# Kernel tuning notes

Hardware: AMD Instinct MI355X
Metric: run time of the kernel (lower is better)

The kernel has to match this reference:

```python
import jax, jax.numpy as jnp
import numpy as np

B, T, C, H = 4, 2048, 1024, 16


def setup_inputs() -> dict:
    key = jax.random.key(0)
    k0, k1, k2 = jax.random.split(key, 3)
    s = C ** -0.5
    return {
        "x": jax.random.normal(k0, (B, T, C), jnp.float32),
        "Wqkv": jax.random.normal(k1, (C, 3 * C), jnp.float32) * s,
        "bqkv": jnp.zeros((3 * C,), jnp.float32),
        "Wo": jax.random.normal(k2, (C, C), jnp.float32) * s,
        "bo": jnp.zeros((C,), jnp.float32),
        "decoder": 1,
    }


def reference(x, Wqkv, bqkv, Wo, bo, decoder):
    Bx, Tx, Cx = x.shape
    d = Cx // H  # head dim
    qkv = x @ Wqkv + bqkv  # [B,T,3C]
    q, k, v = jnp.split(qkv, 3, axis=-1)
    q = q.reshape(Bx, Tx, H, d).transpose(0, 2, 1, 3)  # [B,H,T,d]
    k = k.reshape(Bx, Tx, H, d).transpose(0, 2, 1, 3)
    v = v.reshape(Bx, Tx, H, d).transpose(0, 2, 1, 3)
    # Source: qk / embd_dim**(-0.5)  ==  qk * sqrt(embd_dim)  (faithful quirk)
    scale = jnp.asarray(Cx ** 0.5, x.dtype)
    qk = jnp.einsum("bhqd,bhkd->bhqk", q, k) * scale  # [B,H,T,T]
    if decoder:  # decoder is a Python int constant
        tril = jnp.tril(jnp.ones((Tx, Tx), bool))
        qk = jnp.where(tril, qk, -jnp.inf)
    attn = jax.nn.softmax(qk, axis=-1)
    out = jnp.einsum("bhqk,bhkd->bhqd", attn, v)  # [B,H,T,d]
    out = out.transpose(0, 2, 1, 3).reshape(Bx, Tx, Cx)
    return out @ Wo + bo
```

## Files before the change

kernel.cpp:

```cpp
#include <hip/hip_runtime.h>
#include <cstdint>
#include <cstddef>

#define T_SEQ 2048
#define CEMB  1024
#define NHEAD 16
#define DHEAD 64

#define QSCALE 46.1662413084468f

typedef __attribute__((ext_vector_type(8))) short bf16x8;
typedef __attribute__((ext_vector_type(4))) float f32x4;

static __device__ __forceinline__ unsigned short f2bf(float x) {
    unsigned u = __builtin_bit_cast(unsigned, x);
    unsigned r = (u + 0x7FFFu + ((u >> 16) & 1u)) >> 16;
    return (unsigned short)r;
}
static __device__ __forceinline__ float bf2f(unsigned short b) {
    unsigned u = ((unsigned)b) << 16;
    return __builtin_bit_cast(float, u);
}

static __device__ __forceinline__ void gload16(const short* gsrc, short* ldsbase) {
    __builtin_amdgcn_global_load_lds(
        (const __attribute__((address_space(1))) void*)gsrc,
        (__attribute__((address_space(3))) void*)ldsbase, 16, 0, 0);
}

__global__ __launch_bounds__(256) void gemm_qk_kernel(
    const float* __restrict__ Af,
    const short* __restrict__ Bh, const short* __restrict__ Bl,
    const float* __restrict__ bias,
    short* __restrict__ Chi, short* __restrict__ Clo, int K)
{
    __shared__ __align__(16) short smem[16384];

    const int tid = threadIdx.x;
    const int w = tid >> 6, l = tid & 63;
    const int lr = l & 15, lg = l >> 4;
    const int wr = w >> 1, wc = w & 1;
    const int row0 = blockIdx.y * 128;
    const int col0 = blockIdx.x * 128;

    f32x4 acc[4][4];
    #pragma unroll
    for (int mt = 0; mt < 4; ++mt)
        #pragma unroll
        for (int nt = 0; nt < 4; ++nt)
            acc[mt][nt] = (f32x4){0.f, 0.f, 0.f, 0.f};

    const int sB0 = w * 128 + l, sB1 = sB0 + 64;
    const size_t bO0 = (size_t)(col0 + (sB0 & 127)) * K + (sB0 >> 7) * 8;
    const size_t bO1 = (size_t)(col0 + (sB1 & 127)) * K + (sB1 >> 7) * 8;
    const short* gB0  = Bh + bO0;  const short* gB1  = Bh + bO1;
    const short* gBl0 = Bl + bO0;  const short* gBl1 = Bl + bO1;
    short* const dB0 = &smem[4096 + (w * 128) * 8];
    short* const dB1 = &smem[4096 + (w * 128 + 64) * 8];

    const int arow = tid >> 1, ahalf = tid & 1;
    const float* gAf = Af + (size_t)(row0 + arow) * K + ahalf * 16;

    for (int kt = 0; kt < K; kt += 32) {
        __syncthreads();
        gload16(gB0 + kt, dB0);
        gload16(gB1 + kt, dB1);
        gload16(gBl0 + kt, dB0 + 8192);
        gload16(gBl1 + kt, dB1 + 8192);
        {
            const float* src = gAf + kt;
            float4 f0 = *(const float4*)(src);
            float4 f1 = *(const float4*)(src + 4);
            float4 f2 = *(const float4*)(src + 8);
            float4 f3 = *(const float4*)(src + 12);
            float xs[16] = {f0.x, f0.y, f0.z, f0.w, f1.x, f1.y, f1.z, f1.w,
                            f2.x, f2.y, f2.z, f2.w, f3.x, f3.y, f3.z, f3.w};
            #pragma unroll
            for (int q = 0; q < 2; ++q) {
                bf16x8 h8, l8;
                #pragma unroll
                for (int e = 0; e < 8; ++e) {
                    float x = xs[q * 8 + e];
                    unsigned u = __builtin_bit_cast(unsigned, x);
                    h8[e] = (short)(unsigned short)(u >> 16);
                    float hf = __builtin_bit_cast(float, u & 0xFFFF0000u);
                    l8[e] = (short)f2bf(x - hf);
                }
                int slot = (ahalf * 2 + q) * 128 + arow;
                *(bf16x8*)&smem[slot * 8] = h8;
                *(bf16x8*)&smem[8192 + slot * 8] = l8;
            }
        }
        __syncthreads();

        const int ao = (lg * 128 + wr * 64 + lr) * 8;
        const int bo = 4096 + (lg * 128 + wc * 64 + lr) * 8;
        bf16x8 ahf[4], alf[4];
        #pragma unroll
        for (int mt = 0; mt < 4; ++mt) {
            ahf[mt] = *(const bf16x8*)&smem[ao + mt * 128];
            alf[mt] = *(const bf16x8*)&smem[8192 + ao + mt * 128];
        }
        #pragma unroll
        for (int nt = 0; nt < 4; ++nt) {
            bf16x8 bhf = *(const bf16x8*)&smem[bo + nt * 128];
            bf16x8 blf = *(const bf16x8*)&smem[8192 + bo + nt * 128];
            #pragma unroll
            for (int mt = 0; mt < 4; ++mt) {
                acc[mt][nt] = __builtin_amdgcn_mfma_f32_16x16x32_bf16(ahf[mt], bhf, acc[mt][nt], 0, 0, 0);
                acc[mt][nt] = __builtin_amdgcn_mfma_f32_16x16x32_bf16(alf[mt], bhf, acc[mt][nt], 0, 0, 0);
                acc[mt][nt] = __builtin_amdgcn_mfma_f32_16x16x32_bf16(ahf[mt], blf, acc[mt][nt], 0, 0, 0);
            }
        }
    }

    #pragma unroll
    for (int mt = 0; mt < 4; ++mt) {
        #pragma unroll
        for (int r = 0; r < 4; ++r) {
            int m = row0 + wr * 64 + mt * 16 + lg * 4 + r;
            #pragma unroll
            for (int nt = 0; nt < 4; ++nt) {
                int n = col0 + wc * 64 + nt * 16 + lr;
                float v = acc[mt][nt][r] + bias[n];
                if (n < 1024) v *= QSCALE;
                unsigned u = __builtin_bit_cast(unsigned, v);
                Chi[(size_t)m * 2048 + n] = (short)(unsigned short)(u >> 16);
                float hf = __builtin_bit_cast(float, u & 0xFFFF0000u);
                Clo[(size_t)m * 2048 + n] = (short)f2bf(v - hf);
            }
        }
    }
}

__global__ __launch_bounds__(256) void gemm_v_kernel(
    const float* __restrict__ Af, const short* __restrict__ Bh,
    const float* __restrict__ bias, short* __restrict__ vt, int K)
{
    __shared__ __align__(16) short smem[17408];

    const int tid = threadIdx.x;
    const int w = tid >> 6, l = tid & 63;
    const int lr = l & 15, lg = l >> 4;
    const int wr = w >> 1, wc = w & 1;
    const int row0 = blockIdx.y * 128;
    const int col0 = blockIdx.x * 128;

    f32x4 acc[4][4];
    #pragma unroll
    for (int mt = 0; mt < 4; ++mt)
        #pragma unroll
        for (int nt = 0; nt < 4; ++nt)
            acc[mt][nt] = (f32x4){0.f, 0.f, 0.f, 0.f};

    const int sB0 = w * 128 + l, sB1 = sB0 + 64;
    const size_t bO0 = (size_t)(col0 + (sB0 & 127)) * K + (sB0 >> 7) * 8;
    const size_t bO1 = (size_t)(col0 + (sB1 & 127)) * K + (sB1 >> 7) * 8;
    const short* gB0 = Bh + bO0;  const short* gB1 = Bh + bO1;
    short* const dB0 = &smem[4096 + (w * 128) * 8];
    short* const dB1 = &smem[4096 + (w * 128 + 64) * 8];

    const int arow = tid >> 1, ahalf = tid & 1;
    const float* gAf = Af + (size_t)(row0 + arow) * K + ahalf * 16;

    for (int kt = 0; kt < K; kt += 32) {
        __syncthreads();
        gload16(gB0 + kt, dB0);
        gload16(gB1 + kt, dB1);
        {
            const float* src = gAf + kt;
            float4 f0 = *(const float4*)(src);
            float4 f1 = *(const float4*)(src + 4);
            float4 f2 = *(const float4*)(src + 8);
            float4 f3 = *(const float4*)(src + 12);
            float xs[16] = {f0.x, f0.y, f0.z, f0.w, f1.x, f1.y, f1.z, f1.w,
                            f2.x, f2.y, f2.z, f2.w, f3.x, f3.y, f3.z, f3.w};
            #pragma unroll
            for (int q = 0; q < 2; ++q) {
                bf16x8 h8;
                #pragma unroll
                for (int e = 0; e < 8; ++e) h8[e] = (short)f2bf(xs[q * 8 + e]);
                int slot = (ahalf * 2 + q) * 128 + arow;
                *(bf16x8*)&smem[slot * 8] = h8;
            }
        }
        __syncthreads();

        const int ao = (lg * 128 + wr * 64 + lr) * 8;
        const int bo = 4096 + (lg * 128 + wc * 64 + lr) * 8;
        bf16x8 ahf[4];
        #pragma unroll
        for (int mt = 0; mt < 4; ++mt)
            ahf[mt] = *(const bf16x8*)&smem[ao + mt * 128];
        #pragma unroll
        for (int nt = 0; nt < 4; ++nt) {
            bf16x8 bhf = *(const bf16x8*)&smem[bo + nt * 128];
            #pragma unroll
            for (int mt = 0; mt < 4; ++mt)
                acc[mt][nt] = __builtin_amdgcn_mfma_f32_16x16x32_bf16(ahf[mt], bhf, acc[mt][nt], 0, 0, 0);
        }
    }

    __syncthreads();
    #pragma unroll
    for (int mt = 0; mt < 4; ++mt) {
        const int tb = wr * 64 + mt * 16 + lg * 4;
        #pragma unroll
        for (int nt = 0; nt < 4; ++nt) {
            const int nl = wc * 64 + nt * 16 + lr;
            float bv = bias[col0 + nl];
            unsigned u0 = (unsigned)f2bf(acc[mt][nt][0] + bv) |
                          ((unsigned)f2bf(acc[mt][nt][1] + bv) << 16);
            unsigned u1 = (unsigned)f2bf(acc[mt][nt][2] + bv) |
                          ((unsigned)f2bf(acc[mt][nt][3] + bv) << 16);
            uint2 uu; uu.x = u0; uu.y = u1;
            *(uint2*)&smem[nl * 136 + tb] = uu;
        }
    }
    __syncthreads();

    const int b  = row0 >> 11;
    const int t0 = row0 & 2047;
    #pragma unroll
    for (int i = 0; i < 8; ++i) {
        int nl = (tid >> 4) + i * 16;
        int t8 = (tid & 15) * 8;
        bf16x8 vv = *(const bf16x8*)&smem[nl * 136 + t8];
        int n = col0 + nl;
        int hh = n >> 6, d = n & 63;
        short* dst = vt + ((size_t)((b * NHEAD + hh) * DHEAD + d)) * T_SEQ + t0 + t8;
        *(bf16x8*)dst = vv;
    }
}

__global__ __launch_bounds__(256) void gemm_proj_kernel(
    const short* __restrict__ Ah, const short* __restrict__ Bh,
    const float* __restrict__ bias, float* __restrict__ Cout, int K, int ldc)
{
    __shared__ __align__(16) short smem[16384];

    const int tid = threadIdx.x;
    const int w = tid >> 6, l = tid & 63;
    const int lr = l & 15, lg = l >> 4;
    const int wr = w >> 1, wc = w & 1;
    const int row0 = blockIdx.y * 128;
    const int col0 = blockIdx.x * 128;

    f32x4 acc[4][4];
    #pragma unroll
    for (int mt = 0; mt < 4; ++mt)
        #pragma unroll
        for (int nt = 0; nt < 4; ++nt)
            acc[mt][nt] = (f32x4){0.f, 0.f, 0.f, 0.f};

    const int s0 = w * 128 + l, s1 = s0 + 64;
    const size_t aoff0 = (size_t)(row0 + (s0 & 127)) * K + (s0 >> 7) * 8;
    const size_t aoff1 = (size_t)(row0 + (s1 & 127)) * K + (s1 >> 7) * 8;
    const size_t boff0 = (size_t)(col0 + (s0 & 127)) * K + (s0 >> 7) * 8;
    const size_t boff1 = (size_t)(col0 + (s1 & 127)) * K + (s1 >> 7) * 8;
    const short* gA0 = Ah + aoff0;  const short* gA1 = Ah + aoff1;
    const short* gB0 = Bh + boff0;  const short* gB1 = Bh + boff1;
    short* const dA0 = &smem[(w * 128) * 8];
    short* const dA1 = &smem[(w * 128 + 64) * 8];
    short* const dB0 = &smem[4096 + (w * 128) * 8];
    short* const dB1 = &smem[4096 + (w * 128 + 64) * 8];

    #define PSTAGE(buf, kt) do {                      \
        gload16(gA0 + (kt), dA0 + (buf) * 8192);      \
        gload16(gA1 + (kt), dA1 + (buf) * 8192);      \
        gload16(gB0 + (kt), dB0 + (buf) * 8192);      \
        gload16(gB1 + (kt), dB1 + (buf) * 8192);      \
    } while (0)

    const int nkt = K / 32;
    PSTAGE(0, 0);
    for (int ti = 0; ti < nkt; ++ti) {
        if (ti + 1 < nkt) {
            PSTAGE((ti + 1) & 1, (ti + 1) * 32);
            asm volatile("s_waitcnt vmcnt(4)" ::: "memory");
        } else {
            asm volatile("s_waitcnt vmcnt(0)" ::: "memory");
        }
        __builtin_amdgcn_s_barrier();
        __builtin_amdgcn_sched_barrier(0);

        const int sb = (ti & 1) * 8192;
        const int ao = sb + (lg * 128 + wr * 64 + lr) * 8;
        const int bo = sb + 4096 + (lg * 128 + wc * 64 + lr) * 8;
        bf16x8 ahf[4];
        #pragma unroll
        for (int mt = 0; mt < 4; ++mt)
            ahf[mt] = *(const bf16x8*)&smem[ao + mt * 128];
        #pragma unroll
        for (int nt = 0; nt < 4; ++nt) {
            bf16x8 bhf = *(const bf16x8*)&smem[bo + nt * 128];
            #pragma unroll
            for (int mt = 0; mt < 4; ++mt)
                acc[mt][nt] = __builtin_amdgcn_mfma_f32_16x16x32_bf16(ahf[mt], bhf, acc[mt][nt], 0, 0, 0);
        }
        __builtin_amdgcn_sched_barrier(0);
        __builtin_amdgcn_s_barrier();
        __builtin_amdgcn_sched_barrier(0);
    }
    #undef PSTAGE

    #pragma unroll
    for (int mt = 0; mt < 4; ++mt) {
        #pragma unroll
        for (int r = 0; r < 4; ++r) {
            int m = row0 + wr * 64 + mt * 16 + lg * 4 + r;
            #pragma unroll
            for (int nt = 0; nt < 4; ++nt) {
                int n = col0 + wc * 64 + nt * 16 + lr;
                Cout[(size_t)m * ldc + n] = acc[mt][nt][r] + bias[n];
            }
        }
    }
}

__global__ __launch_bounds__(256) void transpose_split_kernel(
    const float* __restrict__ src, int nsrc,
    short* __restrict__ hi, short* __restrict__ lo)
{
    __shared__ float tile[64][68];
    const int tid = threadIdx.x;
    const int n0 = blockIdx.x * 64, k0 = blockIdx.y * 64;
    {
        int kr = tid >> 2, cg = tid & 3;
        const float* s = src + (size_t)(k0 + kr) * nsrc + n0 + cg * 16;
        #pragma unroll
        for (int q = 0; q < 4; ++q) {
            float4 f = *(const float4*)(s + q * 4);
            tile[kr][cg * 16 + q * 4 + 0] = f.x;
            tile[kr][cg * 16 + q * 4 + 1] = f.y;
            tile[kr][cg * 16 + q * 4 + 2] = f.z;
            tile[kr][cg * 16 + q * 4 + 3] = f.w;
        }
    }
    __syncthreads();
    {
        int nr = tid >> 2, kg = tid & 3;
        int n = n0 + nr;
        bf16x8 h0, h1, lo0, lo1;
        #pragma unroll
        for (int e = 0; e < 8; ++e) {
            float a = tile[kg * 16 + e][nr];
            float b = tile[kg * 16 + 8 + e][nr];
            unsigned short ha = f2bf(a), hb = f2bf(b);
            h0[e] = (short)ha; h1[e] = (short)hb;
            lo0[e] = (short)f2bf(a - bf2f(ha));
            lo1[e] = (short)f2bf(b - bf2f(hb));
        }
        short* dh = hi + (size_t)n * 1024 + k0 + kg * 16;
        *(bf16x8*)dh = h0;
        *(bf16x8*)(dh + 8) = h1;
        if (lo) {
            short* dl = lo + (size_t)n * 1024 + k0 + kg * 16;
            *(bf16x8*)dl = lo0;
            *(bf16x8*)(dl + 8) = lo1;
        }
    }
}

__global__ __launch_bounds__(256) void attn_mfma_kernel(
    const short* __restrict__ qkhi, const short* __restrict__ qklo,
    const short* __restrict__ vt, short* __restrict__ ctxb)
{
    __shared__ __align__(16) short smem[20480];

    const int tid = threadIdx.x;
    const int w = tid >> 6, l = tid & 63;
    const int lr = l & 15, lg = l >> 4;

    const int bid = blockIdx.x;
    const int p  = bid >> 6;
    const int bh = bid & 63;
    const int h = bh & 15, b = bh >> 4;
    const size_t bT = (size_t)b * T_SEQ;

    const int g0 = w * 128 + l, g1 = g0 + 64;
    const int rg0 = g0 >> 3, rg1 = g1 >> 3;
    const int sc0 = (g0 & 7) ^ (rg0 & 7), sc1 = (g1 & 7) ^ (rg1 & 7);
    short* const dK0 = &smem[(w * 128) * 8];
    short* const dK1 = &smem[(w * 128 + 64) * 8];

    const size_t koff0 = (bT + rg0) * 2048 + 1024 + h * DHEAD + sc0 * 8;
    const size_t koff1 = (bT + rg1) * 2048 + 1024 + h * DHEAD + sc1 * 8;
    const short* const pKh0 = qkhi + koff0;
    const short* const pKh1 = qkhi + koff1;
    const short* const pKl0 = qklo + koff0;
    const short* const pKl1 = qklo + koff1;
    const short* const pV0 = vt + ((size_t)((b * NHEAD + h) * DHEAD) + rg0) * T_SEQ + sc0 * 8;
    const short* const pV1 = vt + ((size_t)((b * NHEAD + h) * DHEAD) + rg1) * T_SEQ + sc1 * 8;

    const int psBase = 16384 + w * 1024;
    const int pwChunk = (lg >> 1);
    const int pwIntra = (lg & 1) * 4;

    for (int half = 0; half < 2; ++half) {
        const int xi = half ? (31 - p) : p;
        const int qw = xi * 64 + w * 16;
        const int nsteps = xi + 1;

        __syncthreads();

        bf16x8 qhi[2], qlo[2];
        #pragma unroll
        for (int kk = 0; kk < 2; ++kk) {
            size_t off = (bT + qw + lr) * 2048 + h * DHEAD + kk * 32 + lg * 8;
            qhi[kk] = *(const bf16x8*)(qkhi + off);
            qlo[kk] = *(const bf16x8*)(qklo + off);
        }
        __builtin_amdgcn_sched_barrier(0);

        gload16(pKh0, dK0);
        gload16(pKh1, dK1);
        gload16(pKl0, dK0 + 4096);
        gload16(pKl1, dK1 + 4096);
        gload16(pV0, dK0 + 8192);
        gload16(pV1, dK1 + 8192);
        {
            int j1 = (nsteps > 1) ? 64 : 0;
            gload16(pV0 + j1, dK0 + 12288);
            gload16(pV1 + j1, dK1 + 12288);
        }

        f32x4 O[4];
        #pragma unroll
        for (int dt = 0; dt < 4; ++dt)
            O[dt] = (f32x4){0.f, 0.f, 0.f, 0.f};
        float mrow = -3.0e38f;
        float lrow = 0.f;

        for (int t = 0; t < nsteps; ++t) {
            const int j0 = t * 64;
            asm volatile("s_waitcnt vmcnt(2)" ::: "memory");
            __builtin_amdgcn_s_barrier();
            __builtin_amdgcn_sched_barrier(0);
            const int vbase = 8192 + (t & 1) * 4096;

            f32x4 St[4];
            __builtin_amdgcn_s_setprio(1);
            #pragma unroll
            for (int ct = 0; ct < 4; ++ct) {
                f32x4 s = (f32x4){0.f, 0.f, 0.f, 0.f};
                #pragma unroll
                for (int kk = 0; kk < 2; ++kk) {
                    int j  = ct * 16 + lr;
                    int ck = kk * 4 + lg;
                    int idx = j * 64 + ((ck ^ (j & 7)) << 3);
                    bf16x8 kh8 = *(bf16x8*)&smem[idx];
                    bf16x8 kl8 = *(bf16x8*)&smem[4096 + idx];
                    s = __builtin_amdgcn_mfma_f32_16x16x32_bf16(kh8, qhi[kk], s, 0, 0, 0);
                    s = __builtin_amdgcn_mfma_f32_16x16x32_bf16(kh8, qlo[kk], s, 0, 0, 0);
                    s = __builtin_amdgcn_mfma_f32_16x16x32_bf16(kl8, qhi[kk], s, 0, 0, 0);
                }
                St[ct] = s;
            }
            __builtin_amdgcn_s_setprio(0);
            #pragma unroll
            for (int ct = 0; ct < 4; ++ct) {
                if (j0 + ct * 16 + 15 > qw) {
                    #pragma unroll
                    for (int r = 0; r < 4; ++r) {
                        int jabs = j0 + ct * 16 + lg * 4 + r;
                        St[ct][r] = (jabs <= qw + lr) ? St[ct][r] : -3.0e38f;
                    }
                }
            }

            float tm = fmaxf(fmaxf(fmaxf(St[0][0], St[0][1]), fmaxf(St[0][2], St[0][3])),
                             fmaxf(fmaxf(St[1][0], St[1][1]), fmaxf(St[1][2], St[1][3])));
            tm = fmaxf(tm, fmaxf(fmaxf(fmaxf(St[2][0], St[2][1]), fmaxf(St[2][2], St[2][3])),
                                 fmaxf(fmaxf(St[3][0], St[3][1]), fmaxf(St[3][2], St[3][3]))));
            tm = fmaxf(tm, __shfl_xor(tm, 16));
            tm = fmaxf(tm, __shfl_xor(tm, 32));

            if (__any(tm > mrow)) {
                float mnew  = fmaxf(mrow, tm);
                float alpha = __builtin_amdgcn_exp2f(mrow - mnew);
                mrow = mnew;
                lrow *= alpha;
                #pragma unroll
                for (int r = 0; r < 4; ++r) {
                    float aO = __shfl(alpha, lg * 4 + r);
                    #pragma unroll
                    for (int dt = 0; dt < 4; ++dt)
                        O[dt][r] *= aO;
                }
            }

            #pragma unroll
            for (int ct = 0; ct < 4; ++ct) {
                float p0 = __builtin_amdgcn_exp2f(St[ct][0] - mrow);
                float p1 = __builtin_amdgcn_exp2f(St[ct][1] - mrow);
                float p2 = __builtin_amdgcn_exp2f(St[ct][2] - mrow);
                float p3 = __builtin_amdgcn_exp2f(St[ct][3] - mrow);
                lrow += (p0 + p1) + (p2 + p3);
                unsigned u0 = (__builtin_bit_cast(unsigned, p0) >> 16) |
                              (__builtin_bit_cast(unsigned, p1) & 0xFFFF0000u);
                unsigned u1 = (__builtin_bit_cast(unsigned, p2) >> 16) |
                              (__builtin_bit_cast(unsigned, p3) & 0xFFFF0000u);
                int chunk = ct * 2 + pwChunk;
                int sidx = psBase + lr * 64 + ((chunk ^ (lr & 7)) << 3) + pwIntra;
                uint2 uu; uu.x = u0; uu.y = u1;
                *(uint2*)&smem[sidx] = uu;
            }

            __builtin_amdgcn_wave_barrier();

            bf16x8 pa[2];
            #pragma unroll
            for (int jk = 0; jk < 2; ++jk) {
                int ck = jk * 4 + lg;
                pa[jk] = *(bf16x8*)&smem[psBase + lr * 64 + ((ck ^ (lr & 7)) << 3)];
            }
            __builtin_amdgcn_s_setprio(1);
            #pragma unroll
            for (int dt = 0; dt < 4; ++dt) {
                #pragma unroll
                for (int jk = 0; jk < 2; ++jk) {
                    int d  = dt * 16 + lr;
                    int ck = jk * 4 + lg;
                    bf16x8 vb = *(bf16x8*)&smem[vbase + d * 64 + ((ck ^ (d & 7)) << 3)];
                    O[dt] = __builtin_amdgcn_mfma_f32_16x16x32_bf16(pa[jk], vb, O[dt], 0, 0, 0);
                }
            }
            __builtin_amdgcn_s_setprio(0);

            __builtin_amdgcn_sched_barrier(0);
            __builtin_amdgcn_s_barrier();
            __builtin_amdgcn_sched_barrier(0);

            if (t + 1 < nsteps) {
                size_t ko = (size_t)(t + 1) * 131072;
                gload16(pKh0 + ko, dK0);
                gload16(pKh1 + ko, dK1);
                gload16(pKl0 + ko, dK0 + 4096);
                gload16(pKl1 + ko, dK1 + 4096);
                int jv = (t + 2 < nsteps) ? (t + 2) : (nsteps - 1);
                short* const dV = &smem[8192 + (t & 1) * 4096];
                gload16(pV0 + jv * 64, dV + (w * 128) * 8);
                gload16(pV1 + jv * 64, dV + (w * 128 + 64) * 8);
            }
        }

        float lsum = lrow + __shfl_xor(lrow, 16);
        lsum += __shfl_xor(lsum, 32);
        #pragma unroll
        for (int r = 0; r < 4; ++r) {
            float lO = __shfl(lsum, lg * 4 + r);
            float inv = 1.0f / lO;
            int row = qw + lg * 4 + r;
            #pragma unroll
            for (int dt = 0; dt < 4; ++dt) {
                int col = h * DHEAD + dt * 16 + lr;
                ctxb[(size_t)(b * T_SEQ + row) * CEMB + col] = (short)f2bf(O[dt][r] * inv);
            }
        }
    }
}

extern "C" void kernel_launch(void* const* d_in, const int* in_sizes, int n_in,
                              void* d_out, int out_size, void* d_ws, size_t ws_size,
                              hipStream_t stream)
{
    const float* x    = (const float*)d_in[0];
    const float* Wqkv = (const float*)d_in[1];
    const float* bqkv = (const float*)d_in[2];
    const float* Wo   = (const float*)d_in[3];
    const float* bo   = (const float*)d_in[4];
    float* out = (float*)d_out;

    char* ws = (char*)d_ws;
    short* qkhi = (short*)ws;
    short* qklo = (short*)(ws + (size_t)(32u << 20));
    short* Vt   = (short*)(ws + (size_t)(64u << 20));
    short* ctxb = (short*)(ws + (size_t)(80u << 20));
    short* WhiT = (short*)(ws + (size_t)(96u << 20));
    short* WloT = (short*)(ws + (size_t)(102u << 20));
    short* WoT  = (short*)(ws + (size_t)(108u << 20));

    transpose_split_kernel<<<dim3(48, 16), 256, 0, stream>>>(Wqkv, 3 * CEMB, WhiT, WloT);
    transpose_split_kernel<<<dim3(16, 16), 256, 0, stream>>>(Wo, CEMB, WoT, nullptr);

    gemm_qk_kernel<<<dim3(16, 64), 256, 0, stream>>>(
        x, WhiT, WloT, bqkv, qkhi, qklo, CEMB);

    gemm_v_kernel<<<dim3(8, 64), 256, 0, stream>>>(
        x, WhiT + (size_t)2048 * 1024, bqkv + 2048, Vt, CEMB);

    attn_mfma_kernel<<<dim3(1024), 256, 0, stream>>>(qkhi, qklo, Vt, ctxb);

    gemm_proj_kernel<<<dim3(8, 64), 256, 0, stream>>>(
        ctxb, WoT, bo, out, CEMB, CEMB);
}
```

Before: 329.6 us.

## Double-buffer B tiles and prefetch A registers in QKV projection GEMM

Restructures the QKV GEMM main loop so the next K-slice of the B operand (hi/lo bf16) is loaded into a second LDS buffer, and the next A floats into registers, while the current slice is being multiplied. Explicit vmcnt/lgkmcnt waits and raw s_barrier calls replace the __syncthreads pair, and s_setprio raises wave priority around the MFMA block. This is meant to hide global-load latency behind MFMA work. In exchange it uses more LDS (48KB instead of 32KB), which may cut occupancy, and it relies on hand-counted waitcnt values being correct.

```diff
diff --git a/kernel.cpp b/kernel.cpp
--- a/kernel.cpp
+++ b/kernel.cpp
@@ -34,7 +34,7 @@
     const float* __restrict__ bias,
     short* __restrict__ Chi, short* __restrict__ Clo, int K)
 {
-    __shared__ __align__(16) short smem[16384];
+    __shared__ __align__(16) short smem[24576];
 
     const int tid = threadIdx.x;
     const int w = tid >> 6, l = tid & 63;
@@ -55,26 +55,38 @@
     const size_t bO1 = (size_t)(col0 + (sB1 & 127)) * K + (sB1 >> 7) * 8;
     const short* gB0  = Bh + bO0;  const short* gB1  = Bh + bO1;
     const short* gBl0 = Bl + bO0;  const short* gBl1 = Bl + bO1;
-    short* const dB0 = &smem[4096 + (w * 128) * 8];
-    short* const dB1 = &smem[4096 + (w * 128 + 64) * 8];
+    short* const dB0base = &smem[8192 + (w * 128) * 8];
+    short* const dB1base = &smem[8192 + (w * 128 + 64) * 8];
 
     const int arow = tid >> 1, ahalf = tid & 1;
     const float* gAf = Af + (size_t)(row0 + arow) * K + ahalf * 16;
 
-    for (int kt = 0; kt < K; kt += 32) {
-        __syncthreads();
-        gload16(gB0 + kt, dB0);
-        gload16(gB1 + kt, dB1);
-        gload16(gBl0 + kt, dB0 + 8192);
-        gload16(gBl1 + kt, dB1 + 8192);
+    float4 fa0, fa1, fa2, fa3;
+    #define LOADA(kt) do {                                                  \
+        const float* s_ = gAf + (kt);                                       \
+        fa0 = *(const float4*)(s_);                                         \
+        fa1 = *(const float4*)(s_ + 4);                                     \
+        fa2 = *(const float4*)(s_ + 8);                                     \
+        fa3 = *(const float4*)(s_ + 12);                                    \
+    } while (0)
+    #define STAGEB(buf, kt) do {                                            \
+        gload16(gB0 + (kt),  dB0base + (buf) * 8192);                       \
+        gload16(gB1 + (kt),  dB1base + (buf) * 8192);                       \
+        gload16(gBl0 + (kt), dB0base + (buf) * 8192 + 4096);                \
+        gload16(gBl1 + (kt), dB1base + (buf) * 8192 + 4096);                \
+    } while (0)
+
+    LOADA(0);
+    STAGEB(0, 0);
+
+    const int nkt = K / 32;
+    for (int ti = 0; ti < nkt; ++ti) {
+        asm volatile("s_waitcnt vmcnt(4)" ::: "memory");
+        __builtin_amdgcn_sched_barrier(0);
+
         {
-            const float* src = gAf + kt;
-            float4 f0 = *(const float4*)(src);
-            float4 f1 = *(const float4*)(src + 4);
-            float4 f2 = *(const float4*)(src + 8);
-            float4 f3 = *(const float4*)(src + 12);
-            float xs[16] = {f0.x, f0.y, f0.z, f0.w, f1.x, f1.y, f1.z, f1.w,
-                            f2.x, f2.y, f2.z, f2.w, f3.x, f3.y, f3.z, f3.w};
+            float xs[16] = {fa0.x, fa0.y, fa0.z, fa0.w, fa1.x, fa1.y, fa1.z, fa1.w,
+                            fa2.x, fa2.y, fa2.z, fa2.w, fa3.x, fa3.y, fa3.z, fa3.w};
             #pragma unroll
             for (int q = 0; q < 2; ++q) {
                 bf16x8 h8, l8;
@@ -88,23 +100,35 @@
                 }
                 int slot = (ahalf * 2 + q) * 128 + arow;
                 *(bf16x8*)&smem[slot * 8] = h8;
-                *(bf16x8*)&smem[8192 + slot * 8] = l8;
-            }
-        }
-        __syncthreads();
-
+                *(bf16x8*)&smem[4096 + slot * 8] = l8;
+            }
+        }
+
+        if (ti + 1 < nkt) {
+            LOADA((ti + 1) * 32);
+            STAGEB((ti + 1) & 1, (ti + 1) * 32);
+            asm volatile("s_waitcnt vmcnt(8)" ::: "memory");
+        } else {
+            asm volatile("s_waitcnt vmcnt(0)" ::: "memory");
+        }
+        asm volatile("s_waitcnt lgkmcnt(0)" ::: "memory");
+        __builtin_amdgcn_s_barrier();
+        __builtin_amdgcn_sched_barrier(0);
+
+        const int sbB = 8192 + (ti & 1) * 8192;
         const int ao = (lg * 128 + wr * 64 + lr) * 8;
-        const int bo = 4096 + (lg * 128 + wc * 64 + lr) * 8;
+        const int bo = sbB + (lg * 128 + wc * 64 + lr) * 8;
         bf16x8 ahf[4], alf[4];
         #pragma unroll
         for (int mt = 0; mt < 4; ++mt) {
             ahf[mt] = *(const bf16x8*)&smem[ao + mt * 128];
-            alf[mt] = *(const bf16x8*)&smem[8192 + ao + mt * 128];
-        }
+            alf[mt] = *(const bf16x8*)&smem[4096 + ao + mt * 128];
+        }
+        __builtin_amdgcn_s_setprio(1);
         #pragma unroll
         for (int nt = 0; nt < 4; ++nt) {
             bf16x8 bhf = *(const bf16x8*)&smem[bo + nt * 128];
-            bf16x8 blf = *(const bf16x8*)&smem[8192 + bo + nt * 128];
+            bf16x8 blf = *(const bf16x8*)&smem[4096 + bo + nt * 128];
             #pragma unroll
             for (int mt = 0; mt < 4; ++mt) {
                 acc[mt][nt] = __builtin_amdgcn_mfma_f32_16x16x32_bf16(ahf[mt], bhf, acc[mt][nt], 0, 0, 0);
@@ -112,7 +136,13 @@
                 acc[mt][nt] = __builtin_amdgcn_mfma_f32_16x16x32_bf16(ahf[mt], blf, acc[mt][nt], 0, 0, 0);
             }
         }
-    }
+        __builtin_amdgcn_s_setprio(0);
+        __builtin_amdgcn_sched_barrier(0);
+        __builtin_amdgcn_s_barrier();
+        __builtin_amdgcn_sched_barrier(0);
+    }
+    #undef LOADA
+    #undef STAGEB
 
     #pragma unroll
     for (int mt = 0; mt < 4; ++mt) {
```

After: 335.4 us. About the same (+1.8%).

## Merge QK and V projection GEMMs and prefetch K earlier in attention

Applied to the files above, without the earlier changes.

Fuses the separate QK (hi/lo split) and V projection GEMMs into one launch. Blocks whose columns fall in the V range take a single-bf16 path with a transposed V store, which removes a kernel launch and the tail gap between the two GEMMs. In the attention loop, the next K tile prefetch is now issued right after the QK^T MFMAs, behind an extra barrier, so it overlaps with softmax and the PV product. The cost is one more workgroup barrier per step and divergent block types inside the fused GEMM. V blocks also now build A with truncation rather than round-to-nearest bf16.

```diff
diff --git a/kernel.cpp b/kernel.cpp
--- a/kernel.cpp
+++ b/kernel.cpp
@@ -28,13 +28,14 @@
         (__attribute__((address_space(3))) void*)ldsbase, 16, 0, 0);
 }
 
-__global__ __launch_bounds__(256) void gemm_qk_kernel(
+__global__ __launch_bounds__(256) void gemm_qkv_kernel(
     const float* __restrict__ Af,
     const short* __restrict__ Bh, const short* __restrict__ Bl,
     const float* __restrict__ bias,
-    short* __restrict__ Chi, short* __restrict__ Clo, int K)
+    short* __restrict__ Chi, short* __restrict__ Clo,
+    short* __restrict__ vt, int K)
 {
-    __shared__ __align__(16) short smem[16384];
+    __shared__ __align__(16) short smem[17408];
 
     const int tid = threadIdx.x;
     const int w = tid >> 6, l = tid & 63;
@@ -42,6 +43,7 @@
     const int wr = w >> 1, wc = w & 1;
     const int row0 = blockIdx.y * 128;
     const int col0 = blockIdx.x * 128;
+    const bool isV = (col0 >= 2048);
 
     f32x4 acc[4][4];
     #pragma unroll
@@ -65,8 +67,10 @@
         __syncthreads();
         gload16(gB0 + kt, dB0);
         gload16(gB1 + kt, dB1);
-        gload16(gBl0 + kt, dB0 + 8192);
-        gload16(gBl1 + kt, dB1 + 8192);
+        if (!isV) {
+            gload16(gBl0 + kt, dB0 + 8192);
+            gload16(gBl1 + kt, dB1 + 8192);
+        }
         {
             const float* src = gAf + kt;
             float4 f0 = *(const float4*)(src);
@@ -97,139 +101,85 @@
         const int bo = 4096 + (lg * 128 + wc * 64 + lr) * 8;
         bf16x8 ahf[4], alf[4];
         #pragma unroll
-        for (int mt = 0; mt < 4; ++mt) {
-            ahf[mt] = *(const bf16x8*)&smem[ao + mt * 128];
-            alf[mt] = *(const bf16x8*)&smem[8192 + ao + mt * 128];
-        }
-        #pragma unroll
-        for (int nt = 0; nt < 4; ++nt) {
-            bf16x8 bhf = *(const bf16x8*)&smem[bo + nt * 128];
-            bf16x8 blf = *(const bf16x8*)&smem[8192 + bo + nt * 128];
-            #pragma unroll
-            for (int mt = 0; mt < 4; ++mt) {
-                acc[mt][nt] = __builtin_amdgcn_mfma_f32_16x16x32_bf16(ahf[mt], bhf, acc[mt][nt], 0, 0, 0);
-                acc[mt][nt] = __builtin_amdgcn_mfma_f32_16x16x32_bf16(alf[mt], bhf, acc[mt][nt], 0, 0, 0);
-                acc[mt][nt] = __builtin_amdgcn_mfma_f32_16x16x32_bf16(ahf[mt], blf, acc[mt][nt], 0, 0, 0);
-            }
-        }
-    }
-
-    #pragma unroll
-    for (int mt = 0; mt < 4; ++mt) {
-        #pragma unroll
-        for (int r = 0; r < 4; ++r) {
-            int m = row0 + wr * 64 + mt * 16 + lg * 4 + r;
-            #pragma unroll
-            for (int nt = 0; nt < 4; ++nt) {
-                int n = col0 + wc * 64 + nt * 16 + lr;
-                float v = acc[mt][nt][r] + bias[n];
-                if (n < 1024) v *= QSCALE;
-                unsigned u = __builtin_bit_cast(unsigned, v);
-                Chi[(size_t)m * 2048 + n] = (short)(unsigned short)(u >> 16);
-                float hf = __builtin_bit_cast(float, u & 0xFFFF0000u);
-                Clo[(size_t)m * 2048 + n] = (short)f2bf(v - hf);
-            }
-        }
-    }
-}
-
-__global__ __launch_bounds__(256) void gemm_v_kernel(
-    const float* __restrict__ Af, const short* __restrict__ Bh,
-    const float* __restrict__ bias, short* __restrict__ vt, int K)
-{
-    __shared__ __align__(16) short smem[17408];
-
-    const int tid = threadIdx.x;
-    const int w = tid >> 6, l = tid & 63;
-    const int lr = l & 15, lg = l >> 4;
-    const int wr = w >> 1, wc = w & 1;
-    const int row0 = blockIdx.y * 128;
-    const int col0 = blockIdx.x * 128;
-
-    f32x4 acc[4][4];
-    #pragma unroll
-    for (int mt = 0; mt < 4; ++mt)
-        #pragma unroll
-        for (int nt = 0; nt < 4; ++nt)
-            acc[mt][nt] = (f32x4){0.f, 0.f, 0.f, 0.f};
-
-    const int sB0 = w * 128 + l, sB1 = sB0 + 64;
-    const size_t bO0 = (size_t)(col0 + (sB0 & 127)) * K + (sB0 >> 7) * 8;
-    const size_t bO1 = (size_t)(col0 + (sB1 & 127)) * K + (sB1 >> 7) * 8;
-    const short* gB0 = Bh + bO0;  const short* gB1 = Bh + bO1;
-    short* const dB0 = &smem[4096 + (w * 128) * 8];
-    short* const dB1 = &smem[4096 + (w * 128 + 64) * 8];
-
-    const int arow = tid >> 1, ahalf = tid & 1;
-    const float* gAf = Af + (size_t)(row0 + arow) * K + ahalf * 16;
-
-    for (int kt = 0; kt < K; kt += 32) {
-        __syncthreads();
-        gload16(gB0 + kt, dB0);
-        gload16(gB1 + kt, dB1);
-        {
-            const float* src = gAf + kt;
-            float4 f0 = *(const float4*)(src);
-            float4 f1 = *(const float4*)(src + 4);
-            float4 f2 = *(const float4*)(src + 8);
-            float4 f3 = *(const float4*)(src + 12);
-            float xs[16] = {f0.x, f0.y, f0.z, f0.w, f1.x, f1.y, f1.z, f1.w,
-                            f2.x, f2.y, f2.z, f2.w, f3.x, f3.y, f3.z, f3.w};
-            #pragma unroll
-            for (int q = 0; q < 2; ++q) {
-                bf16x8 h8;
-                #pragma unroll
-                for (int e = 0; e < 8; ++e) h8[e] = (short)f2bf(xs[q * 8 + e]);
-                int slot = (ahalf * 2 + q) * 128 + arow;
-                *(bf16x8*)&smem[slot * 8] = h8;
-            }
-        }
-        __syncthreads();
-
-        const int ao = (lg * 128 + wr * 64 + lr) * 8;
-        const int bo = 4096 + (lg * 128 + wc * 64 + lr) * 8;
-        bf16x8 ahf[4];
-        #pragma unroll
         for (int mt = 0; mt < 4; ++mt)
             ahf[mt] = *(const bf16x8*)&smem[ao + mt * 128];
-        #pragma unroll
-        for (int nt = 0; nt < 4; ++nt) {
-            bf16x8 bhf = *(const bf16x8*)&smem[bo + nt * 128];
+        if (!isV) {
             #pragma unroll
             for (int mt = 0; mt < 4; ++mt)
-                acc[mt][nt] = __builtin_amdgcn_mfma_f32_16x16x32_bf16(ahf[mt], bhf, acc[mt][nt], 0, 0, 0);
-        }
-    }
-
-    __syncthreads();
-    #pragma unroll
-    for (int mt = 0; mt < 4; ++mt) {
-        const int tb = wr * 64 + mt * 16 + lg * 4;
-        #pragma unroll
-        for (int nt = 0; nt < 4; ++nt) {
-            const int nl = wc * 64 + nt * 16 + lr;
-            float bv = bias[col0 + nl];
-            unsigned u0 = (unsigned)f2bf(acc[mt][nt][0] + bv) |
-                          ((unsigned)f2bf(acc[mt][nt][1] + bv) << 16);
-            unsigned u1 = (unsigned)f2bf(acc[mt][nt][2] + bv) |
-                          ((unsigned)f2bf(acc[mt][nt][3] + bv) << 16);
-            uint2 uu; uu.x = u0; uu.y = u1;
-            *(uint2*)&smem[nl * 136 + tb] = uu;
-        }
-    }
-    __syncthreads();
-
-    const int b  = row0 >> 11;
-    const int t0 = row0 & 2047;
-    #pragma unroll
-    for (int i = 0; i < 8; ++i) {
-        int nl = (tid >> 4) + i * 16;
-        int t8 = (tid & 15) * 8;
-        bf16x8 vv = *(const bf16x8*)&smem[nl * 136 + t8];
-        int n = col0 + nl;
-        int hh = n >> 6, d = n & 63;
-        short* dst = vt + ((size_t)((b * NHEAD + hh) * DHEAD + d)) * T_SEQ + t0 + t8;
-        *(bf16x8*)dst = vv;
+                alf[mt] = *(const bf16x8*)&smem[8192 + ao + mt * 128];
+        }
+        if (!isV) {
+            #pragma unroll
+            for (int nt = 0; nt < 4; ++nt) {
+                bf16x8 bhf = *(const bf16x8*)&smem[bo + nt * 128];
+                bf16x8 blf = *(const bf16x8*)&smem[8192 + bo + nt * 128];
+                #pragma unroll
+                for (int mt = 0; mt < 4; ++mt) {
+                    acc[mt][nt] = __builtin_amdgcn_mfma_f32_16x16x32_bf16(ahf[mt], bhf, acc[mt][nt], 0, 0, 0);
+                    acc[mt][nt] = __builtin_amdgcn_mfma_f32_16x16x32_bf16(alf[mt], bhf, acc[mt][nt], 0, 0, 0);
+                    acc[mt][nt] = __builtin_amdgcn_mfma_f32_16x16x32_bf16(ahf[mt], blf, acc[mt][nt], 0, 0, 0);
+                }
+            }
+        } else {
+            #pragma unroll
+            for (int nt = 0; nt < 4; ++nt) {
+                bf16x8 bhf = *(const bf16x8*)&smem[bo + nt * 128];
+                #pragma unroll
+                for (int mt = 0; mt < 4; ++mt)
+                    acc[mt][nt] = __builtin_amdgcn_mfma_f32_16x16x32_bf16(ahf[mt], bhf, acc[mt][nt], 0, 0, 0);
+            }
+        }
+    }
+
+    if (!isV) {
+        #pragma unroll
+        for (int mt = 0; mt < 4; ++mt) {
+            #pragma unroll
+            for (int r = 0; r < 4; ++r) {
+                int m = row0 + wr * 64 + mt * 16 + lg * 4 + r;
+                #pragma unroll
+                for (int nt = 0; nt < 4; ++nt) {
+                    int n = col0 + wc * 64 + nt * 16 + lr;
+                    float v = acc[mt][nt][r] + bias[n];
+                    if (n < 1024) v *= QSCALE;
+                    unsigned u = __builtin_bit_cast(unsigned, v);
+                    Chi[(size_t)m * 2048 + n] = (short)(unsigned short)(u >> 16);
+                    float hf = __builtin_bit_cast(float, u & 0xFFFF0000u);
+                    Clo[(size_t)m * 2048 + n] = (short)f2bf(v - hf);
+                }
+            }
+        }
+    } else {
+        __syncthreads();
+        #pragma unroll
+        for (int mt = 0; mt < 4; ++mt) {
+            const int tb = wr * 64 + mt * 16 + lg * 4;
+            #pragma unroll
+            for (int nt = 0; nt < 4; ++nt) {
+                const int nl = wc * 64 + nt * 16 + lr;
+                float bv = bias[col0 + nl];
+                unsigned u0 = (unsigned)f2bf(acc[mt][nt][0] + bv) |
+                              ((unsigned)f2bf(acc[mt][nt][1] + bv) << 16);
+                unsigned u1 = (unsigned)f2bf(acc[mt][nt][2] + bv) |
+                              ((unsigned)f2bf(acc[mt][nt][3] + bv) << 16);
+                uint2 uu; uu.x = u0; uu.y = u1;
+                *(uint2*)&smem[nl * 136 + tb] = uu;
+            }
+        }
+        __syncthreads();
+
+        const int b  = row0 >> 11;
+        const int t0 = row0 & 2047;
+        #pragma unroll
+        for (int i = 0; i < 8; ++i) {
+            int nl = (tid >> 4) + i * 16;
+            int t8 = (tid & 15) * 8;
+            bf16x8 vv = *(const bf16x8*)&smem[nl * 136 + t8];
+            int n = col0 + nl - 2048;
+            int hh = n >> 6, d = n & 63;
+            short* dst = vt + ((size_t)((b * NHEAD + hh) * DHEAD + d)) * T_SEQ + t0 + t8;
+            *(bf16x8*)dst = vv;
+        }
     }
 }
 
@@ -458,6 +408,17 @@
                 St[ct] = s;
             }
             __builtin_amdgcn_s_setprio(0);
+            __builtin_amdgcn_sched_barrier(0);
+            __builtin_amdgcn_s_barrier();
+            __builtin_amdgcn_sched_barrier(0);
+            if (t + 1 < nsteps) {
+                size_t ko = (size_t)(t + 1) * 131072;
+                gload16(pKh0 + ko, dK0);
+                gload16(pKh1 + ko, dK1);
+                gload16(pKl0 + ko, dK0 + 4096);
+                gload16(pKl1 + ko, dK1 + 4096);
+            }
+
             #pragma unroll
             for (int ct = 0; ct < 4; ++ct) {
                 if (j0 + ct * 16 + 15 > qw) {
@@ -533,11 +494,6 @@
             __builtin_amdgcn_sched_barrier(0);
 
             if (t + 1 < nsteps) {
-                size_t ko = (size_t)(t + 1) * 131072;
-                gload16(pKh0 + ko, dK0);
-                gload16(pKh1 + ko, dK1);
-                gload16(pKl0 + ko, dK0 + 4096);
-                gload16(pKl1 + ko, dK1 + 4096);
                 int jv = (t + 2 < nsteps) ? (t + 2) : (nsteps - 1);
                 short* const dV = &smem[8192 + (t & 1) * 4096];
                 gload16(pV0 + jv * 64, dV + (w * 128) * 8);
@@ -584,11 +540,8 @@
     transpose_split_kernel<<<dim3(48, 16), 256, 0, stream>>>(Wqkv, 3 * CEMB, WhiT, WloT);
     transpose_split_kernel<<<dim3(16, 16), 256, 0, stream>>>(Wo, CEMB, WoT, nullptr);
 
-    gemm_qk_kernel<<<dim3(16, 64), 256, 0, stream>>>(
-        x, WhiT, WloT, bqkv, qkhi, qklo, CEMB);
-
-    gemm_v_kernel<<<dim3(8, 64), 256, 0, stream>>>(
-        x, WhiT + (size_t)2048 * 1024, bqkv + 2048, Vt, CEMB);
+    gemm_qkv_kernel<<<dim3(24, 64), 256, 0, stream>>>(
+        x, WhiT, WloT, bqkv, qkhi, qklo, Vt, CEMB);
 
     attn_mfma_kernel<<<dim3(1024), 256, 0, stream>>>(qkhi, qklo, Vt, ctxb);
 
```

After: 343.5 us. 1.04x slower.
